# Optimization experiments

Hardware: AMD Instinct MI355X
Metric: run time of the kernel (lower is better)

Reference implementation:

```python
import jax, jax.numpy as jnp
import numpy as np

NUM_CLASSES = 80


def setup_inputs() -> dict:
    key = jax.random.key(0)
    k1, k2, k3, k4, k5 = jax.random.split(key, 5)
    B, N, C, H, W = 8, 100, 256, 160, 160
    IMG = 1024
    features = jax.random.normal(k1, (B, C, H, W), dtype=jnp.float32)
    # two random corner points per box -> (x1,y1,x2,y2) with x1<=x2, y1<=y2 (image coords)
    pts = jax.random.uniform(k2, (B, N, 2, 2), minval=0.0, maxval=float(IMG))
    lo = jnp.min(pts, axis=2)  # [B,N,2] -> (x1,y1)
    hi = jnp.max(pts, axis=2)  # [B,N,2] -> (x2,y2)
    boxes = jnp.concatenate([lo, hi], axis=-1).astype(jnp.float32)  # [B,N,4]
    gt_classes = jax.random.randint(k3, (B, N), 0, NUM_CLASSES, dtype=jnp.int32)
    neg_y = jax.random.randint(k4, (B, NUM_CLASSES), 0, H, dtype=jnp.int32)
    neg_x = jax.random.randint(k5, (B, NUM_CLASSES), 0, W, dtype=jnp.int32)
    return {"features": features, "boxes": boxes, "gt_classes": gt_classes,
            "neg_y": neg_y, "neg_x": neg_x, "image_h": IMG, "image_w": IMG}


def reference(features, boxes, gt_classes, neg_y, neg_x, image_h, image_w):
    B, C, H, W = features.shape
    N = boxes.shape[1]
    # scale boxes from image coords to feature-map coords, then truncate like .int()
    scale = jnp.array([W / image_w, H / image_h, W / image_w, H / image_h],
                      dtype=features.dtype)
    sb = boxes * scale
    x1 = jnp.clip(jnp.floor(sb[..., 0]), 0, W).astype(jnp.int32)
    y1 = jnp.clip(jnp.floor(sb[..., 1]), 0, H).astype(jnp.int32)
    x2 = jnp.clip(jnp.floor(sb[..., 2]), 0, W).astype(jnp.int32)
    y2 = jnp.clip(jnp.floor(sb[..., 3]), 0, H).astype(jnp.int32)
    valid = (x2 > x1) & (y2 > y1)  # feature_map.numel() > 0 in the original

    # integral image for O(1) per-box region sums (== adaptive_avg_pool2d to 1x1)
    sat = jnp.cumsum(jnp.cumsum(features, axis=2), axis=3)
    sat = jnp.pad(sat, ((0, 0), (0, 0), (1, 0), (1, 0)))  # [B,C,H+1,W+1]

    def gather_corners(sat_b, y1b, x1b, y2b, x2b):
        # sat_b: [C,H+1,W+1]; returns per-box region sums [C,N]
        return (sat_b[:, y2b, x2b] - sat_b[:, y1b, x2b]
                - sat_b[:, y2b, x1b] + sat_b[:, y1b, x1b])

    box_sum = jax.vmap(gather_corners)(sat, y1, x1, y2, x2)  # [B,C,N]
    area = jnp.maximum((x2 - x1) * (y2 - y1), 1).astype(features.dtype)  # [B,N]
    pooled = (box_sum / area[:, None, :]).transpose(0, 2, 1)  # [B,N,C]
    vmask = valid.astype(features.dtype)
    pooled = pooled * vmask[..., None]

    # scatter-mean into per-(image, class) buckets
    seg = (jnp.arange(B, dtype=jnp.int32)[:, None] * NUM_CLASSES + gt_classes).reshape(-1)
    wsum = jax.ops.segment_sum(pooled.reshape(B * N, C), seg,
                               num_segments=B * NUM_CLASSES)  # [B*80,C]
    cnt = jax.ops.segment_sum(vmask.reshape(-1), seg, num_segments=B * NUM_CLASSES)
    mean = (wsum / jnp.maximum(cnt, 1.0)[:, None]).reshape(B, NUM_CLASSES, C)

    # negative sample (random pixel feature) for empty classes
    neg = jax.vmap(lambda f, ys, xs: f[:, ys, xs].T)(features, neg_y, neg_x)  # [B,80,C]
    out = jnp.where(cnt.reshape(B, NUM_CLASSES, 1) > 0, mean, neg)
    return out
```

## Files before the change

### kernel.cpp

```cpp
#include <hip/hip_runtime.h>

namespace {
constexpr int B  = 8;
constexpr int N  = 100;
constexpr int C  = 256;
constexpr int H  = 160;
constexpr int W  = 160;
constexpr int NC = 80;
constexpr int T  = 1024;
constexpr int NW = 16;
constexpr int RPW = H / NW;
constexpr int SCR = 164;
}

__device__ inline float read_dim(const int* p) {
    int i = *p;
    if (i >= 1 && i <= (1 << 26)) return (float)i;
    return __int_as_float(i);
}

#define DPP_ADD(s, ctrl, rmask)                                              \
    s += __int_as_float(__builtin_amdgcn_update_dpp(                          \
        0, __float_as_int(s), (ctrl), (rmask), 0xf, false))

extern "C" __global__ void __launch_bounds__(T)
vpe_kernel(const float* __restrict__ features,
           const float* __restrict__ boxes,
           const int*   __restrict__ gt,
           const int*   __restrict__ neg_y,
           const int*   __restrict__ neg_x,
           const int*   __restrict__ imh_p,
           const int*   __restrict__ imw_p,
           float*       __restrict__ out)
{
    __shared__ float rs[NW * 2 * SCR];
    __shared__ float cls_sum[NC];
    __shared__ int   cls_cnt[NC];
    __shared__ int   bx1m[N], bx2m[N], by1[N], by2[N], bcls[N];
    __shared__ float bwgt[N];

    const int tid  = threadIdx.x;
    const int wave = tid >> 6, lane = tid & 63;
    const int b    = blockIdx.x / C;
    const int c    = blockIdx.x % C;
    const float* plane = features + (size_t)(b * C + c) * (H * W);

    if (tid < NC) { cls_sum[tid] = 0.f; cls_cnt[tid] = 0; }
    __syncthreads();

    if (tid < N) {
        float imw = read_dim(imw_p), imh = read_dim(imh_p);
        float sx = (float)W / imw, sy = (float)H / imh;
        const float* bp = boxes + (size_t)(b * N + tid) * 4;
        int x1 = (int)fminf(fmaxf(floorf(bp[0] * sx), 0.f), (float)W);
        int y1 = (int)fminf(fmaxf(floorf(bp[1] * sy), 0.f), (float)H);
        int x2 = (int)fminf(fmaxf(floorf(bp[2] * sx), 0.f), (float)W);
        int y2 = (int)fminf(fmaxf(floorf(bp[3] * sy), 0.f), (float)H);
        bool valid = (x2 > x1) && (y2 > y1);
        bx1m[tid] = x1 - 1; bx2m[tid] = x2 - 1;
        by1[tid] = y1; by2[tid] = y2;
        int cls = gt[b * N + tid];
        bcls[tid] = valid ? cls : -1;
        bwgt[tid] = 1.f / (float)max((x2 - x1) * (y2 - y1), 1);
        if (valid) atomicAdd(&cls_cnt[cls], 1);
    }
    __syncthreads();
    if (tid < N && bcls[tid] >= 0)
        bwgt[tid] /= (float)max(cls_cnt[bcls[tid]], 1);
    __syncthreads();

    float* buf0 = &rs[(wave * 2 + 0) * SCR];
    float* buf1 = &rs[(wave * 2 + 1) * SCR];
    const int nA = lane, nB = lane + 64;
    const int clsA = bcls[nA];
    const int y1A = by1[nA], y2A = by2[nA], x1A = bx1m[nA], x2A = bx2m[nA];
    const float wA = bwgt[nA];
    int clsB = -1, y1B = 0, y2B = 0, x1B = 0, x2B = 0; float wB = 0.f;
    if (nB < N) {
        clsB = bcls[nB]; y1B = by1[nB]; y2B = by2[nB];
        x1B = bx1m[nB]; x2B = bx2m[nB]; wB = bwgt[nB];
    }

    float accA = 0.f, accB = 0.f;
    const bool ldr = (lane < W / 4);

    const float4 z4 = make_float4(0.f, 0.f, 0.f, 0.f);
    const float4* prow = (const float4*)plane + lane;

    float4 v  = ldr ? prow[(size_t)wave * (W / 4)] : z4;
    float4 vn = (ldr && RPW > 1) ? prow[(size_t)(wave + NW) * (W / 4)] : z4;

    for (int r = 0; r < RPW; ++r) {
        const int y = wave + (r << 4);
        float4 v2 = z4;
        if (r + 2 < RPW && ldr)
            v2 = prow[(size_t)(y + 2 * NW) * (W / 4)];

        float q1 = v.x, q2 = q1 + v.y, q3 = q2 + v.z, t = q3 + v.w;

        float s = t;
        DPP_ADD(s, 0x111, 0xf);
        DPP_ADD(s, 0x112, 0xf);
        DPP_ADD(s, 0x114, 0xf);
        DPP_ADD(s, 0x118, 0xf);
        DPP_ADD(s, 0x142, 0xa);
        DPP_ADD(s, 0x143, 0xc);
        float e = s - t;

        float* cb = (r & 1) ? buf1 : buf0;
        if (ldr)
            ((float4*)cb)[lane] = make_float4(e + q1, e + q2, e + q3, s);
        __builtin_amdgcn_wave_barrier();

        if (clsA >= 0 && y >= y1A && y < y2A) {
            float hi = cb[x2A];
            float lo = (x1A >= 0) ? cb[x1A] : 0.f;
            accA += hi - lo;
        }
        if (clsB >= 0 && y >= y1B && y < y2B) {
            float hi = cb[x2B];
            float lo = (x1B >= 0) ? cb[x1B] : 0.f;
            accB += hi - lo;
        }
        v = vn; vn = v2;
    }

    if (clsA >= 0) atomicAdd(&cls_sum[clsA], accA * wA);
    if (clsB >= 0) atomicAdd(&cls_sum[clsB], accB * wB);
    __syncthreads();

    if (tid < NC) {
        int cnt = cls_cnt[tid];
        float o = (cnt > 0) ? cls_sum[tid]
                            : plane[neg_y[b * NC + tid] * W + neg_x[b * NC + tid]];
        out[((size_t)b * NC + tid) * C + c] = o;
    }
}

extern "C" void kernel_launch(void* const* d_in, const int* in_sizes, int n_in,
                              void* d_out, int out_size, void* d_ws, size_t ws_size,
                              hipStream_t stream) {
    (void)in_sizes; (void)n_in; (void)d_ws; (void)ws_size; (void)out_size;
    vpe_kernel<<<dim3(B * C), dim3(T), 0, stream>>>(
        (const float*)d_in[0],
        (const float*)d_in[1],
        (const int*)d_in[2],
        (const int*)d_in[3],
        (const int*)d_in[4],
        (const int*)d_in[5],
        (const int*)d_in[6],
        (float*)d_out);
}
```

Baseline: 298.0 us.

## Process four channels per block to amortize box setup and deepen prefetch

Each block now handles four channel planes instead of one, so the per-block box decoding, class counting and syncs are shared across four channels. The row loop streams through all four planes and prefetches three rows ahead instead of two, flushing per-channel class sums to a small shared array at each plane boundary. This cuts the grid from 2048 to 512 blocks, which lowers setup overhead but also reduces the number of blocks available to spread across CUs.

Measured after the change: 303.2 us. No clear change (+1.7%).

```diff
diff --git a/kernel.cpp b/kernel.cpp
--- a/kernel.cpp
+++ b/kernel.cpp
@@ -10,7 +10,11 @@
 constexpr int T  = 1024;
 constexpr int NW = 16;
 constexpr int RPW = H / NW;
+constexpr int PC  = 4;
+constexpr int NB  = C / PC;
+constexpr int TR  = PC * RPW;
 constexpr int SCR = 164;
+constexpr int HW  = H * W;
 }
 
 __device__ inline float read_dim(const int* p) {
@@ -34,18 +38,19 @@
            float*       __restrict__ out)
 {
     __shared__ float rs[NW * 2 * SCR];
-    __shared__ float cls_sum[NC];
+    __shared__ float cls_sum[PC][NC];
     __shared__ int   cls_cnt[NC];
     __shared__ int   bx1m[N], bx2m[N], by1[N], by2[N], bcls[N];
     __shared__ float bwgt[N];
 
     const int tid  = threadIdx.x;
     const int wave = tid >> 6, lane = tid & 63;
-    const int b    = blockIdx.x / C;
-    const int c    = blockIdx.x % C;
-    const float* plane = features + (size_t)(b * C + c) * (H * W);
+    const int b    = blockIdx.x / NB;
+    const int c0   = (blockIdx.x % NB) * PC;
+    const float* plane0 = features + (size_t)(b * C + c0) * HW;
 
-    if (tid < NC) { cls_sum[tid] = 0.f; cls_cnt[tid] = 0; }
+    if (tid < PC * NC) ((float*)cls_sum)[tid] = 0.f;
+    if (tid < NC) cls_cnt[tid] = 0;
     __syncthreads();
 
     if (tid < N) {
@@ -83,20 +88,24 @@
 
     float accA = 0.f, accB = 0.f;
     const bool ldr = (lane < W / 4);
+    const float4 z4 = make_float4(0.f, 0.f, 0.f, 0.f);
 
-    const float4 z4 = make_float4(0.f, 0.f, 0.f, 0.f);
-    const float4* prow = (const float4*)plane + lane;
+    auto ld = [&](int ri) -> float4 {
+        if (!ldr || ri >= TR) return z4;
+        int pi = ri / RPW;
+        int y  = wave + ((ri - pi * RPW) << 4);
+        return ((const float4*)(plane0 + (size_t)pi * HW + (size_t)y * W))[lane];
+    };
 
-    float4 v  = ldr ? prow[(size_t)wave * (W / 4)] : z4;
-    float4 vn = (ldr && RPW > 1) ? prow[(size_t)(wave + NW) * (W / 4)] : z4;
+    float4 v0 = ld(0), v1 = ld(1), v2 = ld(2);
 
-    for (int r = 0; r < RPW; ++r) {
-        const int y = wave + (r << 4);
-        float4 v2 = z4;
-        if (r + 2 < RPW && ldr)
-            v2 = prow[(size_t)(y + 2 * NW) * (W / 4)];
+    for (int ri = 0; ri < TR; ++ri) {
+        float4 v3 = ld(ri + 3);
+        const int pi = ri / RPW;
+        const int r  = ri - pi * RPW;
+        const int y  = wave + (r << 4);
 
-        float q1 = v.x, q2 = q1 + v.y, q3 = q2 + v.z, t = q3 + v.w;
+        float q1 = v0.x, q2 = q1 + v0.y, q3 = q2 + v0.z, t = q3 + v0.w;
 
         float s = t;
         DPP_ADD(s, 0x111, 0xf);
@@ -107,7 +116,7 @@
         DPP_ADD(s, 0x143, 0xc);
         float e = s - t;
 
-        float* cb = (r & 1) ? buf1 : buf0;
+        float* cb = (ri & 1) ? buf1 : buf0;
         if (ldr)
             ((float4*)cb)[lane] = make_float4(e + q1, e + q2, e + q3, s);
         __builtin_amdgcn_wave_barrier();
@@ -122,18 +131,23 @@
             float lo = (x1B >= 0) ? cb[x1B] : 0.f;
             accB += hi - lo;
         }
-        v = vn; vn = v2;
+
+        if (r == RPW - 1) {
+            if (clsA >= 0) atomicAdd(&cls_sum[pi][clsA], accA * wA);
+            if (clsB >= 0) atomicAdd(&cls_sum[pi][clsB], accB * wB);
+            accA = 0.f; accB = 0.f;
+        }
+        v0 = v1; v1 = v2; v2 = v3;
     }
-
-    if (clsA >= 0) atomicAdd(&cls_sum[clsA], accA * wA);
-    if (clsB >= 0) atomicAdd(&cls_sum[clsB], accB * wB);
     __syncthreads();
 
-    if (tid < NC) {
-        int cnt = cls_cnt[tid];
-        float o = (cnt > 0) ? cls_sum[tid]
-                            : plane[neg_y[b * NC + tid] * W + neg_x[b * NC + tid]];
-        out[((size_t)b * NC + tid) * C + c] = o;
+    if (tid < PC * NC) {
+        const int pi = tid / NC, cls = tid - pi * NC;
+        const int cnt = cls_cnt[cls];
+        const float* pl = plane0 + (size_t)pi * HW;
+        float o = (cnt > 0) ? cls_sum[pi][cls]
+                            : pl[neg_y[b * NC + cls] * W + neg_x[b * NC + cls]];
+        out[((size_t)b * NC + cls) * C + (c0 + pi)] = o;
     }
 }
 
@@ -141,7 +155,7 @@
                               void* d_out, int out_size, void* d_ws, size_t ws_size,
                               hipStream_t stream) {
     (void)in_sizes; (void)n_in; (void)d_ws; (void)ws_size; (void)out_size;
-    vpe_kernel<<<dim3(B * C), dim3(T), 0, stream>>>(
+    vpe_kernel<<<dim3(B * NB), dim3(T), 0, stream>>>(
         (const float*)d_in[0],
         (const float*)d_in[1],
         (const int*)d_in[2],
```
